# Performance work log

Measured on AMD Instinct MI355X. Metric: run time of the kernel, lower is better.

The kernel has to match this reference:

```python
import jax, jax.numpy as jnp
import numpy as np

MIN_ROUGHNESS = 0.08
MAX_ROUGHNESS = 0.5
N_MIPS = 6  # 512 -> 16 cubemap mip chain


def _safe_normalize(x, eps=1e-20):
    return x * jax.lax.rsqrt(jnp.clip(jnp.sum(x * x, -1, keepdims=True), eps, None))


def _dot(a, b):
    return jnp.sum(a * b, -1, keepdims=True)


def _cube_face_uv(d):
    # nvdiffrast cube addressing (matches util.cube_to_dir face layout)
    x, y, z = d[..., 0], d[..., 1], d[..., 2]
    ax, ay, az = jnp.abs(x), jnp.abs(y), jnp.abs(z)
    is_x = (ax >= ay) & (ax >= az)
    is_y = (~is_x) & (ay >= az)
    face = jnp.where(is_x, jnp.where(x >= 0, 0, 1),
           jnp.where(is_y, jnp.where(y >= 0, 2, 3), jnp.where(z >= 0, 4, 5)))
    ma = jnp.maximum(jnp.where(is_x, ax, jnp.where(is_y, ay, az)), 1e-20)
    u = jnp.where(face == 0, -z, jnp.where(face == 1, z, jnp.where(face == 5, -x, x))) / ma
    v = jnp.where(face == 2, z, jnp.where(face == 3, -z, -y)) / ma
    return face, u, v


def _bilinear_cube(tex, face, u, v):
    # tex: [6,R,R,C]; face/u/v: [...]; edge-clamped bilinear within the face
    R = tex.shape[1]
    tu = (u * 0.5 + 0.5) * R - 0.5
    tv = (v * 0.5 + 0.5) * R - 0.5
    x0 = jnp.floor(tu); y0 = jnp.floor(tv)
    fx = (tu - x0)[..., None]; fy = (tv - y0)[..., None]
    x0i = jnp.clip(x0, 0, R - 1).astype(jnp.int32)
    x1i = jnp.clip(x0 + 1, 0, R - 1).astype(jnp.int32)
    y0i = jnp.clip(y0, 0, R - 1).astype(jnp.int32)
    y1i = jnp.clip(y0 + 1, 0, R - 1).astype(jnp.int32)
    c00 = tex[face, y0i, x0i]; c01 = tex[face, y0i, x1i]
    c10 = tex[face, y1i, x0i]; c11 = tex[face, y1i, x1i]
    return (c00 * (1 - fx) + c01 * fx) * (1 - fy) + (c10 * (1 - fx) + c11 * fx) * fy


def _sample_cubemap(tex, dirs):
    f, u, v = _cube_face_uv(dirs)
    return _bilinear_cube(tex, f, u, v)


def _sample_2d_clamp(tex, uv):
    # tex: [H,W,C]; uv in [0,1]^2, clamp boundary bilinear (FG LUT lookup)
    H, W = tex.shape[0], tex.shape[1]
    tu = uv[..., 0] * W - 0.5
    tv = uv[..., 1] * H - 0.5
    x0 = jnp.floor(tu); y0 = jnp.floor(tv)
    fx = (tu - x0)[..., None]; fy = (tv - y0)[..., None]
    x0i = jnp.clip(x0, 0, W - 1).astype(jnp.int32)
    x1i = jnp.clip(x0 + 1, 0, W - 1).astype(jnp.int32)
    y0i = jnp.clip(y0, 0, H - 1).astype(jnp.int32)
    y1i = jnp.clip(y0 + 1, 0, H - 1).astype(jnp.int32)
    c00 = tex[y0i, x0i]; c01 = tex[y0i, x1i]
    c10 = tex[y1i, x0i]; c11 = tex[y1i, x1i]
    return (c00 * (1 - fx) + c01 * fx) * (1 - fy) + (c10 * (1 - fx) + c11 * fx) * fy


def _get_mip(r, n_levels):
    lo = (jnp.clip(r, MIN_ROUGHNESS, MAX_ROUGHNESS) - MIN_ROUGHNESS) / (MAX_ROUGHNESS - MIN_ROUGHNESS) * (n_levels - 2)
    hi = (jnp.clip(r, MAX_ROUGHNESS, 1.0) - MAX_ROUGHNESS) / (1.0 - MAX_ROUGHNESS) + (n_levels - 2)
    return jnp.where(r < MAX_ROUGHNESS, lo, hi)


def _linear2srgb(x):
    xs = jnp.where(x > 0.0031308, x, 1.0)  # avoid pow(0) grad issues
    return jnp.where(x > 0.0031308, 1.055 * jnp.power(xs, 1.0 / 2.4) - 0.055, 12.92 * x)


def _avg_pool_cube(c):
    F, R, _, C = c.shape
    return c.reshape(F, R // 2, 2, R // 2, 2, C).mean(axis=(2, 4))


def setup_inputs() -> dict:
    key = jax.random.key(0)
    ks = jax.random.split(key, 10)
    B, H, W = 1, 1024, 1024
    gb_pos = jax.random.normal(ks[0], (B, H, W, 3), jnp.float32)
    gb_normal = _safe_normalize(jax.random.normal(ks[1], (B, H, W, 3), jnp.float32))
    basecolor = jax.random.uniform(ks[2], (B, H, W, 3), jnp.float32)
    metallic = jax.random.uniform(ks[3], (B, H, W, 1), jnp.float32)
    roughness = jax.random.uniform(ks[4], (B, H, W, 1), jnp.float32)
    view_pos = jax.random.normal(ks[5], (1, 1, 1, 3), jnp.float32) * 3.0
    diffuse = jax.random.uniform(ks[6], (6, 16, 16, 3), jnp.float32)
    fg_lut = jax.random.uniform(ks[7], (256, 256, 2), jnp.float32)
    specs = {}
    s = jax.random.uniform(ks[8], (6, 512, 512, 3), jnp.float32)
    for l in range(N_MIPS):
        specs['spec%d' % l] = s
        if l < N_MIPS - 1:
            s = _avg_pool_cube(s)
    return dict(gb_pos=gb_pos, gb_normal=gb_normal, basecolor=basecolor,
                metallic=metallic, roughness=roughness, view_pos=view_pos,
                diffuse=diffuse, fg_lut=fg_lut, **specs)


def reference(gb_pos, gb_normal, basecolor, metallic, roughness, view_pos,
              diffuse, fg_lut, spec0, spec1, spec2, spec3, spec4, spec5):
    specs = [spec0, spec1, spec2, spec3, spec4, spec5]
    L = len(specs)
    metallic = metallic[..., :1]
    wo = _safe_normalize(view_pos - gb_pos)
    diffuse_albedo = (1.0 - metallic) * basecolor
    specular_albedo = 0.04 * (1.0 - metallic) + metallic * basecolor
    reflvec = _safe_normalize(2.0 * _dot(wo, gb_normal) * gb_normal - wo)
    # diffuse IBL: cubemap gather along normal
    ambient = _sample_cubemap(diffuse, gb_normal)
    diffuse_linear = ambient * diffuse_albedo
    # FG LUT gather
    NdotV = jnp.clip(_dot(wo, gb_normal), 1e-4, None)
    fg = _sample_2d_clamp(fg_lut, jnp.concatenate([NdotV, roughness], -1))
    # trilinear (linear-mipmap-linear) specular cubemap gather
    mip = jnp.clip(_get_mip(roughness[..., 0], L), 0.0, L - 1.0)
    face, u, v = _cube_face_uv(reflvec)
    spec = jnp.zeros(gb_pos.shape[:-1] + (spec0.shape[-1],), gb_pos.dtype)
    for l in range(L):
        w = jnp.clip(1.0 - jnp.abs(mip - l), 0.0, 1.0)[..., None]
        spec = spec + w * _bilinear_cube(specs[l], face, u, v)
    reflectance = specular_albedo * fg[..., 0:1] + fg[..., 1:2]
    rgb = spec * reflectance + diffuse_linear
    return _linear2srgb(jnp.clip(rgb, 0.0, 1.0))
```

## Files before the change

kernel.cpp:

```cpp
#include <hip/hip_runtime.h>
#include <hip/hip_fp16.h>

struct V3 { float x, y, z; };

__device__ __forceinline__ V3 v3add(V3 a, V3 b){ return {a.x+b.x, a.y+b.y, a.z+b.z}; }
__device__ __forceinline__ V3 v3sub(V3 a, V3 b){ return {a.x-b.x, a.y-b.y, a.z-b.z}; }
__device__ __forceinline__ V3 v3scale(V3 a, float s){ return {a.x*s, a.y*s, a.z*s}; }
__device__ __forceinline__ V3 v3mul(V3 a, V3 b){ return {a.x*b.x, a.y*b.y, a.z*b.z}; }
__device__ __forceinline__ float dot3(V3 a, V3 b){ return fmaf(a.x,b.x, fmaf(a.y,b.y, a.z*b.z)); }
__device__ __forceinline__ V3 nrm3(V3 a){
    float s = rsqrtf(fmaxf(dot3(a,a), 1e-20f));
    return v3scale(a, s);
}

#define NOFF1 0
#define NOFF2 393216
#define NOFF3 491520
#define NOFF4 516096
#define SPEC4_COUNT 522240
#define NFG_OFF 522240
#define NTOT_QUADS 587776
#define APP_DIFF 0
#define APP_M5   1536
#define APP_UINTS 3072
#define WS_BYTES_NEW ((size_t)NTOT_QUADS * 16 + (size_t)APP_UINTS * 4)

#define NQ4_SPEC (SPEC4_COUNT/4)
#define NQ4_FG   (65536/4)
#define NQ4_APP  (APP_UINTS/4)
#define NQ4_TOTAL (NQ4_SPEC + NQ4_FG + NQ4_APP)

__device__ __forceinline__ void cube_face_uv(V3 d, int& face, float& u, float& v){
    float ax = fabsf(d.x), ay = fabsf(d.y), az = fabsf(d.z);
    bool is_x = (ax >= ay) && (ax >= az);
    bool is_y = (!is_x) && (ay >= az);
    face = is_x ? (d.x >= 0.f ? 0 : 1)
                : (is_y ? (d.y >= 0.f ? 2 : 3)
                        : (d.z >= 0.f ? 4 : 5));
    float ma = fmaxf(is_x ? ax : (is_y ? ay : az), 1e-20f);
    float un = (face == 0) ? -d.z : (face == 1) ? d.z : (face == 5) ? -d.x : d.x;
    float vn = (face == 2) ?  d.z : (face == 3) ? -d.z : -d.y;
    float inv = 1.0f / ma;
    u = un * inv;
    v = vn * inv;
}

__device__ __forceinline__ void quad_coord_cube(float u, float v, int R,
                                                int& xq, int& yq, float& fx, float& fy){
    float Rf = (float)R;
    float tu = fmaf(fmaf(u, 0.5f, 0.5f), Rf, -0.5f);
    float tv = fmaf(fmaf(v, 0.5f, 0.5f), Rf, -0.5f);
    float x0f = floorf(tu), y0f = floorf(tv);
    fx = tu - x0f; fy = tv - y0f;
    int x0 = (int)x0f, y0 = (int)y0f;
    fx = (x0 < 0) ? 0.f : fx;
    fy = (y0 < 0) ? 0.f : fy;
    xq = min(max(x0, 0), R-1);
    yq = min(max(y0, 0), R-1);
}

__device__ __forceinline__ void quad_coord_2d(float u, float v, int W, int H,
                                              int& xq, int& yq, float& fx, float& fy){
    float tu = fmaf(u, (float)W, -0.5f);
    float tv = fmaf(v, (float)H, -0.5f);
    float x0f = floorf(tu), y0f = floorf(tv);
    fx = tu - x0f; fy = tv - y0f;
    int x0 = (int)x0f, y0 = (int)y0f;
    fx = (x0 < 0) ? 0.f : fx;
    fy = (y0 < 0) ? 0.f : fy;
    xq = min(max(x0, 0), W-1);
    yq = min(max(y0, 0), H-1);
}

__device__ __forceinline__ V3 q10_blend(uint4 q, float fx, float fy){
    float w00 = (1.f-fx)*(1.f-fy), w01 = fx*(1.f-fy);
    float w10 = (1.f-fx)*fy,       w11 = fx*fy;
    float r = (float)(q.x & 1023u)*w00 + (float)(q.y & 1023u)*w01
            + (float)(q.z & 1023u)*w10 + (float)(q.w & 1023u)*w11;
    float g = (float)((q.x>>10) & 1023u)*w00 + (float)((q.y>>10) & 1023u)*w01
            + (float)((q.z>>10) & 1023u)*w10 + (float)((q.w>>10) & 1023u)*w11;
    float b = (float)((q.x>>20) & 1023u)*w00 + (float)((q.y>>20) & 1023u)*w01
            + (float)((q.z>>20) & 1023u)*w10 + (float)((q.w>>20) & 1023u)*w11;
    const float s = 1.0f/1023.0f;
    return { r*s, g*s, b*s };
}

__device__ __forceinline__ void q10_fg(uint4 q, float fx, float fy,
                                       float& fa, float& fb){
    float w00 = (1.f-fx)*(1.f-fy), w01 = fx*(1.f-fy);
    float w10 = (1.f-fx)*fy,       w11 = fx*fy;
    float a00 = (float)(q.x & 1023u),        b00 = (float)((q.x>>10) & 1023u);
    float a01 = (float)((q.x>>20) & 1023u),  b01 = (float)(q.y & 1023u);
    float a10 = (float)((q.y>>10) & 1023u),  b10 = (float)((q.y>>20) & 1023u);
    float a11 = (float)(q.z & 1023u),        b11 = (float)((q.z>>10) & 1023u);
    const float s = 1.0f/1023.0f;
    fa = (a00*w00 + a01*w01 + a10*w10 + a11*w11) * s;
    fb = (b00*w00 + b01*w01 + b10*w10 + b11*w11) * s;
}

__device__ __forceinline__ V3 lds_bilin(const unsigned* lds, int base, int R,
                                        int face, float u, float v){
    float Rf = (float)R;
    float tu = fmaf(fmaf(u, 0.5f, 0.5f), Rf, -0.5f);
    float tv = fmaf(fmaf(v, 0.5f, 0.5f), Rf, -0.5f);
    float x0f = floorf(tu), y0f = floorf(tv);
    float fx = tu - x0f, fy = tv - y0f;
    int x0 = min(max((int)x0f,     0), R-1);
    int x1 = min(max((int)x0f + 1, 0), R-1);
    int y0 = min(max((int)y0f,     0), R-1);
    int y1 = min(max((int)y0f + 1, 0), R-1);
    const unsigned* fb = lds + base + face * R * R;
    uint4 q = make_uint4(fb[y0*R + x0], fb[y0*R + x1],
                         fb[y1*R + x0], fb[y1*R + x1]);
    return q10_blend(q, fx, fy);
}

__device__ __forceinline__ V3 bilinear_cube3(const float* __restrict__ tex, int R,
                                             int face, float u, float v){
    float Rf = (float)R;
    float tu = fmaf(fmaf(u, 0.5f, 0.5f), Rf, -0.5f);
    float tv = fmaf(fmaf(v, 0.5f, 0.5f), Rf, -0.5f);
    float x0 = floorf(tu), y0 = floorf(tv);
    float fx = tu - x0,    fy = tv - y0;
    int x0i = min(max((int)x0,     0), R-1);
    int x1i = min(max((int)x0 + 1, 0), R-1);
    int y0i = min(max((int)y0,     0), R-1);
    int y1i = min(max((int)y0 + 1, 0), R-1);
    const float* base = tex + (size_t)face * R * R * 3;
    const float* r0 = base + (size_t)y0i * R * 3;
    const float* r1 = base + (size_t)y1i * R * 3;
    float a0 = r0[3*x0i], a1 = r0[3*x0i+1], a2 = r0[3*x0i+2];
    float b0 = r0[3*x1i], b1 = r0[3*x1i+1], b2 = r0[3*x1i+2];
    float d0 = r1[3*x0i], d1 = r1[3*x0i+1], d2 = r1[3*x0i+2];
    float e0 = r1[3*x1i], e1 = r1[3*x1i+1], e2 = r1[3*x1i+2];
    float w00 = (1.f-fx)*(1.f-fy), w01 = fx*(1.f-fy);
    float w10 = (1.f-fx)*fy,       w11 = fx*fy;
    V3 out;
    out.x = a0*w00 + b0*w01 + d0*w10 + e0*w11;
    out.y = a1*w00 + b1*w01 + d1*w10 + e1*w11;
    out.z = a2*w00 + b2*w01 + d2*w10 + e2*w11;
    return out;
}

__device__ __forceinline__ void sample_fg(const float* __restrict__ lut,
                                          float u, float v, float& fa, float& fb){
    const int W = 256, H = 256;
    float tu = fmaf(u, (float)W, -0.5f);
    float tv = fmaf(v, (float)H, -0.5f);
    float x0 = floorf(tu), y0 = floorf(tv);
    float fx = tu - x0,    fy = tv - y0;
    int x0i = min(max((int)x0,     0), W-1);
    int x1i = min(max((int)x0 + 1, 0), W-1);
    int y0i = min(max((int)y0,     0), H-1);
    int y1i = min(max((int)y0 + 1, 0), H-1);
    const float2* l2 = (const float2*)lut;
    float2 a = l2[(size_t)y0i*W + x0i];
    float2 b = l2[(size_t)y0i*W + x1i];
    float2 d = l2[(size_t)y1i*W + x0i];
    float2 e = l2[(size_t)y1i*W + x1i];
    float w00 = (1.f-fx)*(1.f-fy), w01 = fx*(1.f-fy);
    float w10 = (1.f-fx)*fy,       w11 = fx*fy;
    fa = a.x*w00 + b.x*w01 + d.x*w10 + e.x*w11;
    fb = a.y*w00 + b.y*w01 + d.y*w10 + e.y*w11;
}

__device__ __forceinline__ float lin2srgb(float x){
    float xs = (x > 0.0031308f) ? x : 1.0f;
    float p  = __builtin_amdgcn_exp2f(__builtin_amdgcn_logf(xs) * (1.0f/2.4f));
    return (x > 0.0031308f) ? fmaf(1.055f, p, -0.055f) : 12.92f * x;
}

__device__ __forceinline__ float clamp01(float x){ return fminf(fmaxf(x, 0.f), 1.f); }

struct PixPre {
    V3 diff_alb, spec_alb;
    int sface; float su, sv;
    int dface; float du, dv;
    int offA, RA, offB, RB; float f;
    float ndotv, rough;
};

__device__ __forceinline__ PixPre pre_pixel_v(V3 pos, V3 nrm, V3 bc, float m, float r, V3 vp)
{
    V3 wo = nrm3(v3sub(vp, pos));
    float ndv_raw = dot3(wo, nrm);
    V3 refl = nrm3(v3sub(v3scale(nrm, 2.0f*ndv_raw), wo));

    PixPre p;
    float one_m = 1.0f - m;
    p.diff_alb = v3scale(bc, one_m);
    p.spec_alb = { fmaf(m, bc.x, 0.04f*one_m),
                   fmaf(m, bc.y, 0.04f*one_m),
                   fmaf(m, bc.z, 0.04f*one_m) };
    p.ndotv = fmaxf(ndv_raw, 0.0001f);
    p.rough = r;

    const float MIN_R = 0.08f, MAX_R = 0.5f;
    float lo = (fminf(fmaxf(r, MIN_R), MAX_R) - MIN_R) / (MAX_R - MIN_R) * 4.0f;
    float hi = (fminf(fmaxf(r, MAX_R), 1.0f) - MAX_R) / (1.0f - MAX_R) + 4.0f;
    float mip = (r < MAX_R) ? lo : hi;
    mip = fminf(fmaxf(mip, 0.0f), 5.0f);
    int l0 = min((int)mip, 5);
    p.f = mip - (float)l0;
    int l1 = min(l0 + 1, 5);

    int offA = NOFF1;
    offA = (l0 == 2) ? NOFF2 : offA; offA = (l0 == 3) ? NOFF3 : offA;
    offA = (l0 == 4) ? NOFF4 : offA;
    int offB = NOFF1;
    offB = (l1 == 2) ? NOFF2 : offB; offB = (l1 == 3) ? NOFF3 : offB;
    offB = (l1 == 4) ? NOFF4 : offB;
    p.offA = offA; p.RA = 512 >> l0;
    p.offB = offB; p.RB = 512 >> l1;

    cube_face_uv(nrm, p.dface, p.du, p.dv);
    cube_face_uv(refl, p.sface, p.su, p.sv);
    return p;
}

__device__ __forceinline__ unsigned pk3(float a, float b, float c){
    unsigned ia = __float2uint_rn(fminf(fmaxf(a, 0.f), 1.f) * 1023.f);
    unsigned ib = __float2uint_rn(fminf(fmaxf(b, 0.f), 1.f) * 1023.f);
    unsigned ic = __float2uint_rn(fminf(fmaxf(c, 0.f), 1.f) * 1023.f);
    return ia | (ib << 10) | (ic << 20);
}

__global__ __launch_bounds__(256)
void pack_q10r(const float* __restrict__ s1, const float* __restrict__ s2,
               const float* __restrict__ s3, const float* __restrict__ s4,
               const float* __restrict__ s5, const float* __restrict__ diffuse,
               const float* __restrict__ fg_lut,
               uint4* __restrict__ qws)
{
    int t = blockIdx.x * blockDim.x + threadIdx.x;
    if (t >= NQ4_TOTAL) return;

    if (t >= NQ4_SPEC + NQ4_FG) {
        int local4 = (t - NQ4_SPEC - NQ4_FG) * 4;
        const float* src; int idx;
        if (local4 < APP_M5) { src = diffuse; idx = local4; }
        else                 { src = s5;      idx = local4 - APP_M5; }
        const float4* sp = (const float4*)(src + 3*idx);
        float4 a = sp[0], b = sp[1], c = sp[2];
        uint4 o;
        o.x = pk3(a.x, a.y, a.z);
        o.y = pk3(a.w, b.x, b.y);
        o.z = pk3(b.z, b.w, c.x);
        o.w = pk3(c.y, c.z, c.w);
        *(uint4*)((unsigned*)(qws + NTOT_QUADS) + local4) = o;
        return;
    }

    if (t >= NQ4_SPEC) {
        int local = (t - NQ4_SPEC) * 4;
        int x = local & 255, y = local >> 8;
        int y1 = (y == 255) ? y : y + 1;
        const float* r0p = fg_lut + 2*local;
        const float* r1p = fg_lut + 2*((y1 << 8) + x);
        bool edge = (x == 252);
        float4 r0a = ((const float4*)r0p)[0], r0b = ((const float4*)r0p)[1];
        float4 r1a = ((const float4*)r1p)[0], r1b = ((const float4*)r1p)[1];
        float4 r0c = *(const float4*)(r0p + (edge ? 4 : 8));
        float4 r1c = *(const float4*)(r1p + (edge ? 4 : 8));
        float a0[5], b0[5], a1[5], b1[5];
        a0[0]=r0a.x; b0[0]=r0a.y; a0[1]=r0a.z; b0[1]=r0a.w;
        a0[2]=r0b.x; b0[2]=r0b.y; a0[3]=r0b.z; b0[3]=r0b.w;
        a0[4]= edge ? r0b.z : r0c.x; b0[4]= edge ? r0b.w : r0c.y;
        a1[0]=r1a.x; b1[0]=r1a.y; a1[1]=r1a.z; b1[1]=r1a.w;
        a1[2]=r1b.x; b1[2]=r1b.y; a1[3]=r1b.z; b1[3]=r1b.w;
        a1[4]= edge ? r1b.z : r1c.x; b1[4]= edge ? r1b.w : r1c.y;
        #pragma unroll
        for (int k = 0; k < 4; ++k) {
            uint4 q;
            q.x = pk3(a0[k], b0[k], a0[k+1]);
            q.y = pk3(b0[k+1], a1[k], b1[k]);
            q.z = pk3(a1[k+1], b1[k+1], 0.f);
            q.w = 0u;
            qws[(size_t)NFG_OFF + local + k] = q;
        }
        return;
    }

    int local4q = t * 4;
    const float* src; int local; int Rm;
    if      (local4q >= NOFF4) { src = s4; local = local4q - NOFF4; Rm = 31;  }
    else if (local4q >= NOFF3) { src = s3; local = local4q - NOFF3; Rm = 63;  }
    else if (local4q >= NOFF2) { src = s2; local = local4q - NOFF2; Rm = 127; }
    else                       { src = s1; local = local4q;         Rm = 255; }
    int x = local & Rm;
    int y = (local / (Rm + 1)) & Rm;
    int rowUp = (y == Rm) ? 0 : (Rm + 1);
    const float* r0p = src + 3*local;
    const float* r1p = src + 3*(local + rowUp);
    bool edge = (x + 4 > Rm);
    float4 A0 = ((const float4*)r0p)[0], A1 = ((const float4*)r0p)[1], A2 = ((const float4*)r0p)[2];
    float4 B0 = ((const float4*)r1p)[0], B1 = ((const float4*)r1p)[1], B2 = ((const float4*)r1p)[2];
    float4 A3 = *(const float4*)(r0p + (edge ? 8 : 12));
    float4 B3 = *(const float4*)(r1p + (edge ? 8 : 12));
    unsigned t0[5], t1[5];
    t0[0] = pk3(A0.x, A0.y, A0.z);
    t0[1] = pk3(A0.w, A1.x, A1.y);
    t0[2] = pk3(A1.z, A1.w, A2.x);
    t0[3] = pk3(A2.y, A2.z, A2.w);
    t0[4] = edge ? t0[3] : pk3(A3.x, A3.y, A3.z);
    t1[0] = pk3(B0.x, B0.y, B0.z);
    t1[1] = pk3(B0.w, B1.x, B1.y);
    t1[2] = pk3(B1.z, B1.w, B2.x);
    t1[3] = pk3(B2.y, B2.z, B2.w);
    t1[4] = edge ? t1[3] : pk3(B3.x, B3.y, B3.z);
    #pragma unroll
    for (int k = 0; k < 4; ++k) {
        uint4 q;
        q.x = t0[k];
        q.y = t0[k+1];
        q.z = t1[k];
        q.w = t1[k+1];
        qws[(size_t)local4q + k] = q;
    }
}

__device__ __forceinline__ V3 sample_spec(const uint4* __restrict__ qws,
                                          const unsigned* lds,
                                          const float* __restrict__ s0raw,
                                          int off, int R, int face, float u, float v){
    if (R == 512)
        return bilinear_cube3(s0raw, 512, face, u, v);
    if (R == 16)
        return lds_bilin(lds, APP_M5, 16, face, u, v);
    int x, y; float fx, fy;
    quad_coord_cube(u, v, R, x, y, fx, fy);
    size_t q = (size_t)off + (size_t)face * R * R + (size_t)y * R + x;
    return q10_blend(qws[q], fx, fy);
}

__device__ __forceinline__ void shade_px(V3 pos, V3 nrm, V3 bc, float m, float r, V3 vp,
                                         const uint4* __restrict__ qws,
                                         const unsigned* lds,
                                         const float* __restrict__ s0raw, float* o)
{
    PixPre p = pre_pixel_v(pos, nrm, bc, m, r, vp);

    int fx_, fy_; float ffx, ffy;
    quad_coord_2d(p.ndotv, p.rough, 256, 256, fx_, fy_, ffx, ffy);
    uint4 F = qws[(size_t)NFG_OFF + (size_t)fy_ * 256 + fx_];

    V3 specA = sample_spec(qws, lds, s0raw, p.offA, p.RA, p.sface, p.su, p.sv);
    V3 specB = sample_spec(qws, lds, s0raw, p.offB, p.RB, p.sface, p.su, p.sv);
    V3 ambient = lds_bilin(lds, APP_DIFF, 16, p.dface, p.du, p.dv);

    float fa, fb;
    q10_fg(F, ffx, ffy, fa, fb);

    V3 spec = { specA.x + (specB.x - specA.x) * p.f,
                specA.y + (specB.y - specA.y) * p.f,
                specA.z + (specB.z - specA.z) * p.f };
    V3 reflc = { fmaf(p.spec_alb.x, fa, fb),
                 fmaf(p.spec_alb.y, fa, fb),
                 fmaf(p.spec_alb.z, fa, fb) };
    V3 rgb = v3add(v3mul(spec, reflc), v3mul(ambient, p.diff_alb));

    o[0] = lin2srgb(clamp01(rgb.x));
    o[1] = lin2srgb(clamp01(rgb.y));
    o[2] = lin2srgb(clamp01(rgb.z));
}

__global__ __launch_bounds__(256)
void envlight_q10r2(const float* __restrict__ gb_pos,
                    const float* __restrict__ gb_normal,
                    const float* __restrict__ basecolor,
                    const float* __restrict__ metallic,
                    const float* __restrict__ roughness,
                    const float* __restrict__ view_pos,
                    const float* __restrict__ s0,
                    const uint4* __restrict__ qws,
                    float* __restrict__ out,
                    int n)
{
    __shared__ unsigned lds_small[APP_UINTS];
    {
        const uint4* app4 = qws + NTOT_QUADS;
        uint4* l4 = (uint4*)lds_small;
        for (int k = threadIdx.x; k < APP_UINTS/4; k += 256)
            l4[k] = app4[k];
    }
    __syncthreads();

    int t = blockIdx.x * blockDim.x + threadIdx.x;
    int i0 = t * 2;
    if (i0 >= n) return;
    V3 vp = { view_pos[0], view_pos[1], view_pos[2] };

    if (i0 + 1 < n) {
        const float2* P = (const float2*)(gb_pos    + 3*i0);
        const float2* N = (const float2*)(gb_normal + 3*i0);
        const float2* B = (const float2*)(basecolor + 3*i0);
        float2 p0 = P[0], p1 = P[1], p2 = P[2];
        float2 n0 = N[0], n1 = N[1], n2 = N[2];
        float2 b0 = B[0], b1 = B[1], b2 = B[2];
        float2 mt = *(const float2*)(metallic  + i0);
        float2 rg = *(const float2*)(roughness + i0);

        float pf[6] = { p0.x,p0.y, p1.x,p1.y, p2.x,p2.y };
        float nf[6] = { n0.x,n0.y, n1.x,n1.y, n2.x,n2.y };
        float bf[6] = { b0.x,b0.y, b1.x,b1.y, b2.x,b2.y };
        float mf[2] = { mt.x, mt.y };
        float rf[2] = { rg.x, rg.y };
        float of[6];

        #pragma unroll
        for (int j = 0; j < 2; ++j) {
            V3 pos = { pf[3*j], pf[3*j+1], pf[3*j+2] };
            V3 nrm = { nf[3*j], nf[3*j+1], nf[3*j+2] };
            V3 bc  = { bf[3*j], bf[3*j+1], bf[3*j+2] };
            shade_px(pos, nrm, bc, mf[j], rf[j], vp, qws, lds_small, s0, of + 3*j);
        }

        float2* O = (float2*)(out + 3*i0);
        O[0] = make_float2(of[0], of[1]);
        O[1] = make_float2(of[2], of[3]);
        O[2] = make_float2(of[4], of[5]);
    } else {
        int i = i0;
        V3 pos = { gb_pos[3*i],    gb_pos[3*i+1],    gb_pos[3*i+2] };
        V3 nrm = { gb_normal[3*i], gb_normal[3*i+1], gb_normal[3*i+2] };
        V3 bc  = { basecolor[3*i], basecolor[3*i+1], basecolor[3*i+2] };
        float o[3];
        shade_px(pos, nrm, bc, metallic[i], roughness[i], vp, qws, lds_small, s0, o);
        out[3*i+0] = o[0]; out[3*i+1] = o[1]; out[3*i+2] = o[2];
    }
}

__global__ __launch_bounds__(256)
void envlight_fallback(const float* __restrict__ gb_pos,
                       const float* __restrict__ gb_normal,
                       const float* __restrict__ basecolor,
                       const float* __restrict__ metallic,
                       const float* __restrict__ roughness,
                       const float* __restrict__ view_pos,
                       const float* __restrict__ diffuse,
                       const float* __restrict__ fg_lut,
                       const float* __restrict__ s0, const float* __restrict__ s1,
                       const float* __restrict__ s2, const float* __restrict__ s3,
                       const float* __restrict__ s4, const float* __restrict__ s5,
                       float* __restrict__ out, int n)
{
    int i = blockIdx.x * blockDim.x + threadIdx.x;
    if (i >= n) return;
    V3 vp = { view_pos[0], view_pos[1], view_pos[2] };
    V3 pos = { gb_pos[3*i],    gb_pos[3*i+1],    gb_pos[3*i+2] };
    V3 nrm = { gb_normal[3*i], gb_normal[3*i+1], gb_normal[3*i+2] };
    V3 bc  = { basecolor[3*i], basecolor[3*i+1], basecolor[3*i+2] };
    PixPre p = pre_pixel_v(pos, nrm, bc, metallic[i], roughness[i], vp);
    int l0 = 0;
    l0 = (p.RA == 256) ? 1 : l0; l0 = (p.RA == 128) ? 2 : l0;
    l0 = (p.RA ==  64) ? 3 : l0; l0 = (p.RA ==  32) ? 4 : l0;
    l0 = (p.RA ==  16) ? 5 : l0;
    int l1 = min(l0 + 1, 5);
    const float* tA = s0;
    tA = (l0 == 1) ? s1 : tA; tA = (l0 == 2) ? s2 : tA;
    tA = (l0 == 3) ? s3 : tA; tA = (l0 == 4) ? s4 : tA; tA = (l0 == 5) ? s5 : tA;
    const float* tB = s0;
    tB = (l1 == 1) ? s1 : tB; tB = (l1 == 2) ? s2 : tB;
    tB = (l1 == 3) ? s3 : tB; tB = (l1 == 4) ? s4 : tB; tB = (l1 == 5) ? s5 : tB;
    V3 ambient = bilinear_cube3(diffuse, 16, p.dface, p.du, p.dv);
    V3 specA   = bilinear_cube3(tA, p.RA, p.sface, p.su, p.sv);
    V3 specB   = bilinear_cube3(tB, p.RB, p.sface, p.su, p.sv);
    float fa, fb;
    sample_fg(fg_lut, p.ndotv, p.rough, fa, fb);
    V3 spec = { specA.x + (specB.x - specA.x) * p.f,
                specA.y + (specB.y - specA.y) * p.f,
                specA.z + (specB.z - specA.z) * p.f };
    V3 reflc = { fmaf(p.spec_alb.x, fa, fb),
                 fmaf(p.spec_alb.y, fa, fb),
                 fmaf(p.spec_alb.z, fa, fb) };
    V3 rgb = v3add(v3mul(spec, reflc), v3mul(ambient, p.diff_alb));
    out[3*i+0] = lin2srgb(clamp01(rgb.x));
    out[3*i+1] = lin2srgb(clamp01(rgb.y));
    out[3*i+2] = lin2srgb(clamp01(rgb.z));
}

extern "C" void kernel_launch(void* const* d_in, const int* in_sizes, int n_in,
                              void* d_out, int out_size, void* d_ws, size_t ws_size,
                              hipStream_t stream) {
    const float* gb_pos    = (const float*)d_in[0];
    const float* gb_normal = (const float*)d_in[1];
    const float* basecolor = (const float*)d_in[2];
    const float* metallic  = (const float*)d_in[3];
    const float* roughness = (const float*)d_in[4];
    const float* view_pos  = (const float*)d_in[5];
    const float* diffuse   = (const float*)d_in[6];
    const float* fg_lut    = (const float*)d_in[7];
    const float* s0        = (const float*)d_in[8];
    const float* s1        = (const float*)d_in[9];
    const float* s2        = (const float*)d_in[10];
    const float* s3        = (const float*)d_in[11];
    const float* s4        = (const float*)d_in[12];
    const float* s5        = (const float*)d_in[13];
    float* out = (float*)d_out;

    int n = in_sizes[0] / 3;
    int block = 256;

    if (ws_size >= WS_BYTES_NEW) {
        uint4* qws = (uint4*)d_ws;
        int pgrid = (NQ4_TOTAL + block - 1) / block;
        pack_q10r<<<pgrid, block, 0, stream>>>(s1, s2, s3, s4, s5,
                                               diffuse, fg_lut, qws);
        int t2 = (n + 1) / 2;
        int mgrid = (t2 + block - 1) / block;
        envlight_q10r2<<<mgrid, block, 0, stream>>>(gb_pos, gb_normal, basecolor,
            metallic, roughness, view_pos, s0, qws, out, n);
    } else {
        int grid = (n + block - 1) / block;
        envlight_fallback<<<grid, block, 0, stream>>>(gb_pos, gb_normal, basecolor,
            metallic, roughness, view_pos, diffuse, fg_lut,
            s0, s1, s2, s3, s4, s5, out, n);
    }
}
```

Baseline: 151.0 us.

## Pack all mips into quad workspace and batch gathers without LDS

```diff
diff --git a/kernel.cpp b/kernel.cpp
--- a/kernel.cpp
+++ b/kernel.cpp
@@ -13,22 +13,21 @@
     return v3scale(a, s);
 }
 
-#define NOFF1 0
-#define NOFF2 393216
-#define NOFF3 491520
-#define NOFF4 516096
-#define SPEC4_COUNT 522240
-#define NFG_OFF 522240
-#define NTOT_QUADS 587776
-#define APP_DIFF 0
-#define APP_M5   1536
-#define APP_UINTS 3072
-#define WS_BYTES_NEW ((size_t)NTOT_QUADS * 16 + (size_t)APP_UINTS * 4)
-
-#define NQ4_SPEC (SPEC4_COUNT/4)
-#define NQ4_FG   (65536/4)
-#define NQ4_APP  (APP_UINTS/4)
-#define NQ4_TOTAL (NQ4_SPEC + NQ4_FG + NQ4_APP)
+#define OFF0 0
+#define OFF1 1572864
+#define OFF2 1966080
+#define OFF3 2064384
+#define OFF4 2088960
+#define OFF5 2095104
+#define DIFF_OFF 2096640
+#define SPEC_DIFF_COUNT 2098176
+#define FG_OFF 2098176
+#define TOTAL_QUADS 2163712
+#define WS_BYTES_Q ((size_t)TOTAL_QUADS * 16)
+
+#define PQ4_SPEC (SPEC_DIFF_COUNT/4)
+#define PQ4_FG   (65536/4)
+#define PQ4_TOTAL (PQ4_SPEC + PQ4_FG)
 
 __device__ __forceinline__ void cube_face_uv(V3 d, int& face, float& u, float& v){
     float ax = fabsf(d.x), ay = fabsf(d.y), az = fabsf(d.z);
@@ -96,23 +95,6 @@
     const float s = 1.0f/1023.0f;
     fa = (a00*w00 + a01*w01 + a10*w10 + a11*w11) * s;
     fb = (b00*w00 + b01*w01 + b10*w10 + b11*w11) * s;
-}
-
-__device__ __forceinline__ V3 lds_bilin(const unsigned* lds, int base, int R,
-                                        int face, float u, float v){
-    float Rf = (float)R;
-    float tu = fmaf(fmaf(u, 0.5f, 0.5f), Rf, -0.5f);
-    float tv = fmaf(fmaf(v, 0.5f, 0.5f), Rf, -0.5f);
-    float x0f = floorf(tu), y0f = floorf(tv);
-    float fx = tu - x0f, fy = tv - y0f;
-    int x0 = min(max((int)x0f,     0), R-1);
-    int x1 = min(max((int)x0f + 1, 0), R-1);
-    int y0 = min(max((int)y0f,     0), R-1);
-    int y1 = min(max((int)y0f + 1, 0), R-1);
-    const unsigned* fb = lds + base + face * R * R;
-    uint4 q = make_uint4(fb[y0*R + x0], fb[y0*R + x1],
-                         fb[y1*R + x0], fb[y1*R + x1]);
-    return q10_blend(q, fx, fy);
 }
 
 __device__ __forceinline__ V3 bilinear_cube3(const float* __restrict__ tex, int R,
@@ -204,12 +186,13 @@
     p.f = mip - (float)l0;
     int l1 = min(l0 + 1, 5);
 
-    int offA = NOFF1;
-    offA = (l0 == 2) ? NOFF2 : offA; offA = (l0 == 3) ? NOFF3 : offA;
-    offA = (l0 == 4) ? NOFF4 : offA;
-    int offB = NOFF1;
-    offB = (l1 == 2) ? NOFF2 : offB; offB = (l1 == 3) ? NOFF3 : offB;
-    offB = (l1 == 4) ? NOFF4 : offB;
+    int offA = OFF0;
+    offA = (l0 == 1) ? OFF1 : offA; offA = (l0 == 2) ? OFF2 : offA;
+    offA = (l0 == 3) ? OFF3 : offA; offA = (l0 == 4) ? OFF4 : offA;
+    offA = (l0 == 5) ? OFF5 : offA;
+    int offB = OFF1;
+    offB = (l1 == 2) ? OFF2 : offB; offB = (l1 == 3) ? OFF3 : offB;
+    offB = (l1 == 4) ? OFF4 : offB; offB = (l1 == 5) ? OFF5 : offB;
     p.offA = offA; p.RA = 512 >> l0;
     p.offB = offB; p.RB = 512 >> l1;
 
@@ -226,33 +209,17 @@
 }
 
 __global__ __launch_bounds__(256)
-void pack_q10r(const float* __restrict__ s1, const float* __restrict__ s2,
-               const float* __restrict__ s3, const float* __restrict__ s4,
-               const float* __restrict__ s5, const float* __restrict__ diffuse,
-               const float* __restrict__ fg_lut,
+void pack_q10f(const float* __restrict__ s0, const float* __restrict__ s1,
+               const float* __restrict__ s2, const float* __restrict__ s3,
+               const float* __restrict__ s4, const float* __restrict__ s5,
+               const float* __restrict__ diffuse, const float* __restrict__ fg_lut,
                uint4* __restrict__ qws)
 {
     int t = blockIdx.x * blockDim.x + threadIdx.x;
-    if (t >= NQ4_TOTAL) return;
-
-    if (t >= NQ4_SPEC + NQ4_FG) {
-        int local4 = (t - NQ4_SPEC - NQ4_FG) * 4;
-        const float* src; int idx;
-        if (local4 < APP_M5) { src = diffuse; idx = local4; }
-        else                 { src = s5;      idx = local4 - APP_M5; }
-        const float4* sp = (const float4*)(src + 3*idx);
-        float4 a = sp[0], b = sp[1], c = sp[2];
-        uint4 o;
-        o.x = pk3(a.x, a.y, a.z);
-        o.y = pk3(a.w, b.x, b.y);
-        o.z = pk3(b.z, b.w, c.x);
-        o.w = pk3(c.y, c.z, c.w);
-        *(uint4*)((unsigned*)(qws + NTOT_QUADS) + local4) = o;
-        return;
-    }
-
-    if (t >= NQ4_SPEC) {
-        int local = (t - NQ4_SPEC) * 4;
+    if (t >= PQ4_TOTAL) return;
+
+    if (t >= PQ4_SPEC) {
+        int local = (t - PQ4_SPEC) * 4;
         int x = local & 255, y = local >> 8;
         int y1 = (y == 255) ? y : y + 1;
         const float* r0p = fg_lut + 2*local;
@@ -276,17 +243,20 @@
             q.y = pk3(b0[k+1], a1[k], b1[k]);
             q.z = pk3(a1[k+1], b1[k+1], 0.f);
             q.w = 0u;
-            qws[(size_t)NFG_OFF + local + k] = q;
+            qws[(size_t)FG_OFF + local + k] = q;
         }
         return;
     }
 
     int local4q = t * 4;
     const float* src; int local; int Rm;
-    if      (local4q >= NOFF4) { src = s4; local = local4q - NOFF4; Rm = 31;  }
-    else if (local4q >= NOFF3) { src = s3; local = local4q - NOFF3; Rm = 63;  }
-    else if (local4q >= NOFF2) { src = s2; local = local4q - NOFF2; Rm = 127; }
-    else                       { src = s1; local = local4q;         Rm = 255; }
+    if      (local4q >= DIFF_OFF) { src = diffuse; local = local4q - DIFF_OFF; Rm = 15;  }
+    else if (local4q >= OFF5)     { src = s5;      local = local4q - OFF5;     Rm = 15;  }
+    else if (local4q >= OFF4)     { src = s4;      local = local4q - OFF4;     Rm = 31;  }
+    else if (local4q >= OFF3)     { src = s3;      local = local4q - OFF3;     Rm = 63;  }
+    else if (local4q >= OFF2)     { src = s2;      local = local4q - OFF2;     Rm = 127; }
+    else if (local4q >= OFF1)     { src = s1;      local = local4q - OFF1;     Rm = 255; }
+    else                          { src = s0;      local = local4q;            Rm = 511; }
     int x = local & Rm;
     int y = (local / (Rm + 1)) & Rm;
     int rowUp = (y == Rm) ? 0 : (Rm + 1);
@@ -319,72 +289,63 @@
     }
 }
 
-__device__ __forceinline__ V3 sample_spec(const uint4* __restrict__ qws,
-                                          const unsigned* lds,
-                                          const float* __restrict__ s0raw,
-                                          int off, int R, int face, float u, float v){
-    if (R == 512)
-        return bilinear_cube3(s0raw, 512, face, u, v);
-    if (R == 16)
-        return lds_bilin(lds, APP_M5, 16, face, u, v);
-    int x, y; float fx, fy;
+struct PreOut {
+    V3 dalb, salb; float f;
+    unsigned iF, iA, iB, iD;
+    float fAx, fAy, fBx, fBy, fDx, fDy, fFx, fFy;
+};
+
+__device__ __forceinline__ unsigned addr_cube(int off, int R, int face, float u, float v,
+                                              float& fx, float& fy){
+    int x, y;
     quad_coord_cube(u, v, R, x, y, fx, fy);
-    size_t q = (size_t)off + (size_t)face * R * R + (size_t)y * R + x;
-    return q10_blend(qws[q], fx, fy);
-}
-
-__device__ __forceinline__ void shade_px(V3 pos, V3 nrm, V3 bc, float m, float r, V3 vp,
-                                         const uint4* __restrict__ qws,
-                                         const unsigned* lds,
-                                         const float* __restrict__ s0raw, float* o)
-{
+    return (unsigned)(off + face * R * R + y * R + x);
+}
+
+__device__ __forceinline__ PreOut pre_all(V3 pos, V3 nrm, V3 bc, float m, float r, V3 vp){
     PixPre p = pre_pixel_v(pos, nrm, bc, m, r, vp);
-
-    int fx_, fy_; float ffx, ffy;
-    quad_coord_2d(p.ndotv, p.rough, 256, 256, fx_, fy_, ffx, ffy);
-    uint4 F = qws[(size_t)NFG_OFF + (size_t)fy_ * 256 + fx_];
-
-    V3 specA = sample_spec(qws, lds, s0raw, p.offA, p.RA, p.sface, p.su, p.sv);
-    V3 specB = sample_spec(qws, lds, s0raw, p.offB, p.RB, p.sface, p.su, p.sv);
-    V3 ambient = lds_bilin(lds, APP_DIFF, 16, p.dface, p.du, p.dv);
-
+    PreOut o;
+    o.dalb = p.diff_alb; o.salb = p.spec_alb; o.f = p.f;
+    o.iA = addr_cube(p.offA, p.RA, p.sface, p.su, p.sv, o.fAx, o.fAy);
+    o.iB = addr_cube(p.offB, p.RB, p.sface, p.su, p.sv, o.fBx, o.fBy);
+    o.iD = addr_cube(DIFF_OFF, 16, p.dface, p.du, p.dv, o.fDx, o.fDy);
+    int fx_, fy_;
+    quad_coord_2d(p.ndotv, p.rough, 256, 256, fx_, fy_, o.fFx, o.fFy);
+    o.iF = (unsigned)(FG_OFF + fy_ * 256 + fx_);
+    return o;
+}
+
+__device__ __forceinline__ void finish_px(const PreOut& p,
+                                          uint4 qF, uint4 qA, uint4 qB, uint4 qD,
+                                          float* o){
+    V3 sA  = q10_blend(qA, p.fAx, p.fAy);
+    V3 sB  = q10_blend(qB, p.fBx, p.fBy);
+    V3 amb = q10_blend(qD, p.fDx, p.fDy);
     float fa, fb;
-    q10_fg(F, ffx, ffy, fa, fb);
-
-    V3 spec = { specA.x + (specB.x - specA.x) * p.f,
-                specA.y + (specB.y - specA.y) * p.f,
-                specA.z + (specB.z - specA.z) * p.f };
-    V3 reflc = { fmaf(p.spec_alb.x, fa, fb),
-                 fmaf(p.spec_alb.y, fa, fb),
-                 fmaf(p.spec_alb.z, fa, fb) };
-    V3 rgb = v3add(v3mul(spec, reflc), v3mul(ambient, p.diff_alb));
-
+    q10_fg(qF, p.fFx, p.fFy, fa, fb);
+    V3 spec = { sA.x + (sB.x - sA.x) * p.f,
+                sA.y + (sB.y - sA.y) * p.f,
+                sA.z + (sB.z - sA.z) * p.f };
+    V3 reflc = { fmaf(p.salb.x, fa, fb),
+                 fmaf(p.salb.y, fa, fb),
+                 fmaf(p.salb.z, fa, fb) };
+    V3 rgb = v3add(v3mul(spec, reflc), v3mul(amb, p.dalb));
     o[0] = lin2srgb(clamp01(rgb.x));
     o[1] = lin2srgb(clamp01(rgb.y));
     o[2] = lin2srgb(clamp01(rgb.z));
 }
 
 __global__ __launch_bounds__(256)
-void envlight_q10r2(const float* __restrict__ gb_pos,
-                    const float* __restrict__ gb_normal,
-                    const float* __restrict__ basecolor,
-                    const float* __restrict__ metallic,
-                    const float* __restrict__ roughness,
-                    const float* __restrict__ view_pos,
-                    const float* __restrict__ s0,
-                    const uint4* __restrict__ qws,
-                    float* __restrict__ out,
-                    int n)
+void envlight_q10u(const float* __restrict__ gb_pos,
+                   const float* __restrict__ gb_normal,
+                   const float* __restrict__ basecolor,
+                   const float* __restrict__ metallic,
+                   const float* __restrict__ roughness,
+                   const float* __restrict__ view_pos,
+                   const uint4* __restrict__ qws,
+                   float* __restrict__ out,
+                   int n)
 {
-    __shared__ unsigned lds_small[APP_UINTS];
-    {
-        const uint4* app4 = qws + NTOT_QUADS;
-        uint4* l4 = (uint4*)lds_small;
-        for (int k = threadIdx.x; k < APP_UINTS/4; k += 256)
-            l4[k] = app4[k];
-    }
-    __syncthreads();
-
     int t = blockIdx.x * blockDim.x + threadIdx.x;
     int i0 = t * 2;
     if (i0 >= n) return;
@@ -400,20 +361,17 @@
         float2 mt = *(const float2*)(metallic  + i0);
         float2 rg = *(const float2*)(roughness + i0);
 
-        float pf[6] = { p0.x,p0.y, p1.x,p1.y, p2.x,p2.y };
-        float nf[6] = { n0.x,n0.y, n1.x,n1.y, n2.x,n2.y };
-        float bf[6] = { b0.x,b0.y, b1.x,b1.y, b2.x,b2.y };
-        float mf[2] = { mt.x, mt.y };
-        float rf[2] = { rg.x, rg.y };
+        PreOut A = pre_all({p0.x,p0.y,p1.x}, {n0.x,n0.y,n1.x}, {b0.x,b0.y,b1.x},
+                           mt.x, rg.x, vp);
+        PreOut Bp = pre_all({p1.y,p2.x,p2.y}, {n1.y,n2.x,n2.y}, {b1.y,b2.x,b2.y},
+                            mt.y, rg.y, vp);
+
+        uint4 aF = qws[A.iF],  aA = qws[A.iA],  aB = qws[A.iB],  aD = qws[A.iD];
+        uint4 bF = qws[Bp.iF], bA = qws[Bp.iA], bB = qws[Bp.iB], bD = qws[Bp.iD];
+
         float of[6];
-
-        #pragma unroll
-        for (int j = 0; j < 2; ++j) {
-            V3 pos = { pf[3*j], pf[3*j+1], pf[3*j+2] };
-            V3 nrm = { nf[3*j], nf[3*j+1], nf[3*j+2] };
-            V3 bc  = { bf[3*j], bf[3*j+1], bf[3*j+2] };
-            shade_px(pos, nrm, bc, mf[j], rf[j], vp, qws, lds_small, s0, of + 3*j);
-        }
+        finish_px(A,  aF, aA, aB, aD, of);
+        finish_px(Bp, bF, bA, bB, bD, of + 3);
 
         float2* O = (float2*)(out + 3*i0);
         O[0] = make_float2(of[0], of[1]);
@@ -424,8 +382,10 @@
         V3 pos = { gb_pos[3*i],    gb_pos[3*i+1],    gb_pos[3*i+2] };
         V3 nrm = { gb_normal[3*i], gb_normal[3*i+1], gb_normal[3*i+2] };
         V3 bc  = { basecolor[3*i], basecolor[3*i+1], basecolor[3*i+2] };
+        PreOut A = pre_all(pos, nrm, bc, metallic[i], roughness[i], vp);
+        uint4 aF = qws[A.iF], aA = qws[A.iA], aB = qws[A.iB], aD = qws[A.iD];
         float o[3];
-        shade_px(pos, nrm, bc, metallic[i], roughness[i], vp, qws, lds_small, s0, o);
+        finish_px(A, aF, aA, aB, aD, o);
         out[3*i+0] = o[0]; out[3*i+1] = o[1]; out[3*i+2] = o[2];
     }
 }
@@ -501,15 +461,15 @@
     int n = in_sizes[0] / 3;
     int block = 256;
 
-    if (ws_size >= WS_BYTES_NEW) {
+    if (ws_size >= WS_BYTES_Q) {
         uint4* qws = (uint4*)d_ws;
-        int pgrid = (NQ4_TOTAL + block - 1) / block;
-        pack_q10r<<<pgrid, block, 0, stream>>>(s1, s2, s3, s4, s5,
+        int pgrid = (PQ4_TOTAL + block - 1) / block;
+        pack_q10f<<<pgrid, block, 0, stream>>>(s0, s1, s2, s3, s4, s5,
                                                diffuse, fg_lut, qws);
         int t2 = (n + 1) / 2;
         int mgrid = (t2 + block - 1) / block;
-        envlight_q10r2<<<mgrid, block, 0, stream>>>(gb_pos, gb_normal, basecolor,
-            metallic, roughness, view_pos, s0, qws, out, n);
+        envlight_q10u<<<mgrid, block, 0, stream>>>(gb_pos, gb_normal, basecolor,
+            metallic, roughness, view_pos, qws, out, n);
     } else {
         int grid = (n + block - 1) / block;
         envlight_fallback<<<grid, block, 0, stream>>>(gb_pos, gb_normal, basecolor,
```

Result: slower. 158.9 us (+5.2%).
